# Optimization experiments

Measured on AMD Instinct MI355X. Metric: run time of the kernel, lower is better.

Reference implementation:

```python
import jax, jax.numpy as jnp
import numpy as np

B, S, C, H = 2, 2048, 512, 16
D = C // H  # 32
SQRT_DIM = float(np.sqrt(C))  # module scales by sqrt(in_channels), not sqrt(dim)


def setup_inputs() -> dict:
    key = jax.random.key(0)
    ks = jax.random.split(key, 16)
    sc = 1.0 / np.sqrt(C)
    f32 = jnp.float32
    return {
        "q": jax.random.normal(ks[0], (B, S, C), f32),
        "k": jax.random.normal(ks[1], (B, S, C), f32),
        "v": jax.random.normal(ks[2], (B, S, C), f32),
        "pos_embedding": jax.random.normal(ks[3], (B, S, C), f32),
        "Wq": jax.random.normal(ks[4], (C, C), f32) * sc,
        "bq": jnp.zeros((C,), f32),
        "Wk": jax.random.normal(ks[5], (C, C), f32) * sc,
        "bk": jnp.zeros((C,), f32),
        "Wv": jax.random.normal(ks[6], (C, C), f32) * sc,
        "bv": jnp.zeros((C,), f32),
        "Wp": jax.random.normal(ks[7], (C, C), f32) * sc,  # pos_proj has no bias
        "u_bias": jax.random.normal(ks[8], (H, D), f32) * 0.1,
        "v_bias": jax.random.normal(ks[9], (H, D), f32) * 0.1,
        "Wo": jax.random.normal(ks[10], (C, C), f32) * sc,
        "bo": jnp.zeros((C,), f32),
    }


def _skew(pos_score):
    # Transformer-XL pad-shift trick: [B,H,S1,S2] -> relative-shifted scores
    b, h, s1, s2 = pos_score.shape
    zeros = jnp.zeros((b, h, s1, 1), pos_score.dtype)
    padded = jnp.concatenate([zeros, pos_score], axis=-1)  # [b,h,s1,s2+1]
    padded = padded.reshape(b, h, s2 + 1, s1)
    return padded[:, :, 1:].reshape(b, h, s1, s2)


def reference(q, k, v, pos_embedding, Wq, bq, Wk, bk, Wv, bv, Wp, u_bias, v_bias, Wo, bo):
    query = (q @ Wq.T + bq).reshape(B, S, H, D)      # [B,S,H,D]
    key_ = (k @ Wk.T + bk).reshape(B, S, H, D)
    value = (v @ Wv.T + bv).reshape(B, S, H, D)
    pos = (pos_embedding @ Wp.T).reshape(B, S, H, D)
    content = jnp.einsum('bshd,bthd->bhst', query + u_bias, key_)   # [B,H,S,S]
    pos_score = _skew(jnp.einsum('bshd,bthd->bhst', query + v_bias, pos))
    score = (content + pos_score) / SQRT_DIM
    attn = jax.nn.softmax(score, axis=-1)            # dropout_p=0 (eval)
    context = jnp.einsum('bhst,bthd->bshd', attn, value).reshape(B, S, C)
    return context @ Wo.T + bo
```

## Files before the change

### kernel.cpp

```cpp
#include <hip/hip_runtime.h>
#include <math.h>

#define S_ 2048
#define C_ 512
#define H_ 16
#define D_ 32
#define B_ 2
#define M_ (B_ * S_)
#define RSCALE 0.04419417382415922f

typedef __attribute__((ext_vector_type(8))) short bf16x8;
typedef __attribute__((ext_vector_type(4))) float f32x4;

__device__ inline unsigned short f2bf(float f) {
  unsigned u = __builtin_bit_cast(unsigned, f);
  u += 0x7FFFu + ((u >> 16) & 1u);
  return (unsigned short)(u >> 16);
}

__global__ __launch_bounds__(256) void split_x(
    const float* __restrict__ q, const float* __restrict__ k,
    const float* __restrict__ v, const float* __restrict__ pe,
    short* __restrict__ xh, short* __restrict__ xl) {
  const int z = blockIdx.y;
  const float* src = z == 0 ? q : z == 1 ? k : z == 2 ? v : pe;
  const size_t off = (size_t)z * M_ * C_;
  const size_t i = ((size_t)blockIdx.x * 256 + threadIdx.x) * 4;
  float4 f = *(const float4*)(src + i);
  float ff[4] = {f.x, f.y, f.z, f.w};
  ushort4 hv, lv;
  unsigned short* ph = (unsigned short*)&hv;
  unsigned short* pl = (unsigned short*)&lv;
#pragma unroll
  for (int e = 0; e < 4; ++e) {
    unsigned u = __builtin_bit_cast(unsigned, ff[e]);
    unsigned hi = u & 0xffff0000u;
    ph[e] = (unsigned short)(hi >> 16);
    pl[e] = f2bf(ff[e] - __builtin_bit_cast(float, hi));
  }
  *(ushort4*)(xh + off + i) = hv;
  *(ushort4*)(xl + off + i) = lv;
}

__global__ __launch_bounds__(256) void split_w(
    const float* __restrict__ w0, const float* __restrict__ w1,
    const float* __restrict__ w2, const float* __restrict__ w3,
    const float* __restrict__ w4, short* __restrict__ wh,
    short* __restrict__ wl) {
  const int z = blockIdx.y;
  const float* src = z == 0 ? w0 : z == 1 ? w1 : z == 2 ? w2 : z == 3 ? w3 : w4;
  const size_t off = (size_t)z * C_ * C_;
  const size_t i = ((size_t)blockIdx.x * 256 + threadIdx.x) * 4;
  float4 f = *(const float4*)(src + i);
  float ff[4] = {f.x, f.y, f.z, f.w};
  ushort4 hv, lv;
  unsigned short* ph = (unsigned short*)&hv;
  unsigned short* pl = (unsigned short*)&lv;
#pragma unroll
  for (int e = 0; e < 4; ++e) {
    unsigned u = __builtin_bit_cast(unsigned, ff[e]);
    unsigned hi = u & 0xffff0000u;
    ph[e] = (unsigned short)(hi >> 16);
    pl[e] = f2bf(ff[e] - __builtin_bit_cast(float, hi));
  }
  *(ushort4*)(wh + off + i) = hv;
  *(ushort4*)(wl + off + i) = lv;
}

__device__ __forceinline__ void gemm_core(
    const short* __restrict__ Xh, const short* __restrict__ Xl,
    const short* __restrict__ Wh, const short* __restrict__ Wl,
    const float* bias, const float* bias2, const float* bias3,
    float* __restrict__ Of, short* __restrict__ Ob, short* __restrict__ Ob2,
    int mode) {
  __shared__ __align__(16) short LAh[2][64 * 72];
  __shared__ __align__(16) short LAl[2][64 * 72];
  __shared__ __align__(16) short LBh[2][64 * 72];
  __shared__ __align__(16) short LBl[2][64 * 72];
  const int tid = threadIdx.x;
  const int w = tid >> 6, lane = tid & 63, col = lane & 15, quad = lane >> 4;
  const int bm = blockIdx.y * 64, bn = blockIdx.x * 64;
  const f32x4 zc = {0.f, 0.f, 0.f, 0.f};
  f32x4 acc[4] = {zc, zc, zc, zc};

  uint4 rah[2], ral[2], rbh[2], rbl[2];
  const int r0 = tid >> 3, c0 = (tid & 7) * 8;
  const int r1 = (tid + 256) >> 3, c1 = c0;
#define LOAD_REGS(k0)                                                     \
  {                                                                       \
    rah[0] = *(const uint4*)(Xh + (size_t)(bm + r0) * C_ + (k0) + c0);    \
    ral[0] = *(const uint4*)(Xl + (size_t)(bm + r0) * C_ + (k0) + c0);    \
    rbh[0] = *(const uint4*)(Wh + (size_t)(bn + r0) * C_ + (k0) + c0);    \
    rbl[0] = *(const uint4*)(Wl + (size_t)(bn + r0) * C_ + (k0) + c0);    \
    rah[1] = *(const uint4*)(Xh + (size_t)(bm + r1) * C_ + (k0) + c1);    \
    ral[1] = *(const uint4*)(Xl + (size_t)(bm + r1) * C_ + (k0) + c1);    \
    rbh[1] = *(const uint4*)(Wh + (size_t)(bn + r1) * C_ + (k0) + c1);    \
    rbl[1] = *(const uint4*)(Wl + (size_t)(bn + r1) * C_ + (k0) + c1);    \
  }
#define STORE_LDS(buf)                                                    \
  {                                                                       \
    *(uint4*)&LAh[buf][r0 * 72 + c0] = rah[0];                            \
    *(uint4*)&LAl[buf][r0 * 72 + c0] = ral[0];                            \
    *(uint4*)&LBh[buf][r0 * 72 + c0] = rbh[0];                            \
    *(uint4*)&LBl[buf][r0 * 72 + c0] = rbl[0];                            \
    *(uint4*)&LAh[buf][r1 * 72 + c1] = rah[1];                            \
    *(uint4*)&LAl[buf][r1 * 72 + c1] = ral[1];                            \
    *(uint4*)&LBh[buf][r1 * 72 + c1] = rbh[1];                            \
    *(uint4*)&LBl[buf][r1 * 72 + c1] = rbl[1];                            \
  }
  LOAD_REGS(0)
  STORE_LDS(0)
  for (int it = 0; it < 8; ++it) {
    __syncthreads();
    if (it < 7) LOAD_REGS((it + 1) * 64)
    const int buf = it & 1;
#pragma unroll
    for (int ks = 0; ks < 2; ++ks) {
      const int ko = ks * 32 + quad * 8;
      const bf16x8 ah = *(const bf16x8*)&LAh[buf][(16 * w + col) * 72 + ko];
      const bf16x8 al = *(const bf16x8*)&LAl[buf][(16 * w + col) * 72 + ko];
#pragma unroll
      for (int j = 0; j < 4; ++j) {
        const bf16x8 bh = *(const bf16x8*)&LBh[buf][(16 * j + col) * 72 + ko];
        const bf16x8 bl = *(const bf16x8*)&LBl[buf][(16 * j + col) * 72 + ko];
        acc[j] = __builtin_amdgcn_mfma_f32_16x16x32_bf16(ah, bh, acc[j], 0, 0, 0);
        acc[j] = __builtin_amdgcn_mfma_f32_16x16x32_bf16(ah, bl, acc[j], 0, 0, 0);
        acc[j] = __builtin_amdgcn_mfma_f32_16x16x32_bf16(al, bh, acc[j], 0, 0, 0);
      }
    }
    if (it < 7) STORE_LDS(1 - buf)
  }
#undef LOAD_REGS
#undef STORE_LDS
#pragma unroll
  for (int j = 0; j < 4; ++j) {
    const int gn = bn + 16 * j + col;
#pragma unroll
    for (int r = 0; r < 4; ++r) {
      const int gm = bm + 16 * w + quad * 4 + r;
      const float a = acc[j][r];
      if (mode == 0) {
        Of[(size_t)gm * C_ + gn] = a + (bias ? bias[gn] : 0.0f);
      } else if (mode == 1) {
        const int h = gn >> 5, d0 = gn & 31;
        const int bb = gm >> 11, s = gm & (S_ - 1);
        const size_t base = ((size_t)(bb * H_ + h) * S_ + s) * D_ + d0;
        const float val = a + bias[gn];
        Ob[base] = (short)f2bf(val + bias2[gn]);
        Ob2[base] = (short)f2bf(val + bias3[gn]);
      } else if (mode == 2) {
        const int h = gn >> 5, d0 = gn & 31;
        const int bb = gm >> 11, s = gm & (S_ - 1);
        Ob[((size_t)(bb * H_ + h) * S_ + s) * D_ + d0] =
            (short)f2bf(a + (bias ? bias[gn] : 0.0f));
      } else {
        const int h = gn >> 5, d0 = gn & 31;
        const int bb = gm >> 11, s = gm & (S_ - 1);
        Ob[((size_t)(bb * H_ + h) * D_ + d0) * S_ + s] =
            (short)f2bf(a + (bias ? bias[gn] : 0.0f));
      }
    }
  }
}

__global__ __launch_bounds__(256, 2) void proj4(
    const short* __restrict__ XH, const short* __restrict__ XL,
    const short* __restrict__ WH, const short* __restrict__ WL,
    const float* bq, const float* bkk, const float* bvv,
    const float* ub, const float* vb,
    short* QU, short* QV, short* Kb, short* Vt, short* POS) {
  const int z = blockIdx.z;
  const size_t MC = (size_t)M_ * C_, WC = (size_t)C_ * C_;
  const short* xh = XH + z * MC;
  const short* xl = XL + z * MC;
  const short* wh = WH + z * WC;
  const short* wl = WL + z * WC;
  const float* b1 = z == 0 ? bq : z == 1 ? bkk : z == 2 ? bvv : nullptr;
  const int mode = z == 0 ? 1 : z == 2 ? 3 : 2;
  short* ob = z == 0 ? QU : z == 1 ? Kb : z == 2 ? Vt : POS;
  short* ob2 = z == 0 ? QV : nullptr;
  gemm_core(xh, xl, wh, wl, b1, z == 0 ? ub : nullptr, z == 0 ? vb : nullptr,
            nullptr, ob, ob2, mode);
}

__global__ __launch_bounds__(256, 2) void gemm_out(
    const short* __restrict__ CTXh, const short* __restrict__ CTXl,
    const short* __restrict__ WH, const short* __restrict__ WL,
    const float* bo, float* __restrict__ out) {
  const size_t WC = (size_t)C_ * C_;
  gemm_core(CTXh, CTXl, WH + 4 * WC, WL + 4 * WC, bo, nullptr, nullptr,
            out, nullptr, nullptr, 0);
}

__global__ __launch_bounds__(256, 4) void attn_mfma(
    const short* __restrict__ QU, const short* __restrict__ QV,
    const short* __restrict__ Kb, const short* __restrict__ Vt,
    const short* __restrict__ POSb, short* __restrict__ CTXh,
    short* __restrict__ CTXl) {
  __shared__ float PB[64 * 128];
  __shared__ short Pl[64 * 64];
  const int tid = threadIdx.x;
  const int w = tid >> 6;
  const int lane = tid & 63;
  const int col = lane & 15;
  const int quad = lane >> 4;
  const int m0 = blockIdx.x * 64;
  const int bh = blockIdx.y;
  const int b = bh >> 4, h = bh & 15;

  const short* QUh = QU + (size_t)bh * S_ * D_;
  const short* QVh = QV + (size_t)bh * S_ * D_;
  const short* Kh = Kb + (size_t)bh * S_ * D_;
  const short* Vh = Vt + (size_t)bh * D_ * S_;
  const short* Ph = POSb + (size_t)bh * S_ * D_;

  const int arow = m0 + 16 * w + col;
  const bf16x8 aQU = *(const bf16x8*)(QUh + (size_t)arow * D_ + quad * 8);
  const bf16x8 aQVA = *(const bf16x8*)(QVh + (size_t)arow * D_ + quad * 8);
  const bf16x8 aQVB = *(const bf16x8*)(QVh + (size_t)(arow + 1) * D_ + quad * 8);

  const f32x4 zc = {0.f, 0.f, 0.f, 0.f};
  const bf16x8 zb = {0, 0, 0, 0, 0, 0, 0, 0};
  f32x4 ctxa0 = zc, ctxa1 = zc;
  float lpart[4] = {0.f, 0.f, 0.f, 0.f};
  const int mi0 = 16 * w + 4 * quad;

  for (int ch = 0; ch < 32; ++ch) {
    const int n0 = ch * 64;
    const int dnm = n0 - m0;
    f32x4 sc[4];
#pragma unroll
    for (int j = 0; j < 4; ++j) {
      bf16x8 bk = *(const bf16x8*)(Kh + (size_t)(n0 + 16 * j + col) * D_ + quad * 8);
      sc[j] = __builtin_amdgcn_mfma_f32_16x16x32_bf16(aQU, bk, zc, 0, 0, 0);
    }
    if (dnm <= 63) {
      const int tA0 = S_ - 64 + dnm;
#pragma unroll
      for (int j = 0; j < 8; ++j) {
        const int t = tA0 + 16 * j + col;
        bf16x8 bp = *(const bf16x8*)(Ph + (long)t * D_ + quad * 8);
        if (t >= S_) bp = zb;
        f32x4 c = __builtin_amdgcn_mfma_f32_16x16x32_bf16(aQVA, bp, zc, 0, 0, 0);
#pragma unroll
        for (int r = 0; r < 4; ++r) {
          const int mi = mi0 + r;
          const int cc = (16 * j + col) ^ (((mi & 4) << 2) ^ ((mi & 3) << 3));
          PB[mi * 128 + cc] = c[r];
        }
      }
      __syncthreads();
#pragma unroll
      for (int j = 0; j < 4; ++j)
#pragma unroll
        for (int r = 0; r < 4; ++r) {
          const int mi = mi0 + r;
          const int nj = 16 * j + col;
          if (dnm + nj - mi <= 0) {
            const int idx = (nj - mi + 63) ^ (((mi & 4) << 2) ^ ((mi & 3) << 3));
            sc[j][r] += PB[mi * 128 + idx];
          }
        }
    }
    if (dnm >= -61) {
      __syncthreads();
      const int tB0 = dnm - 65;
#pragma unroll
      for (int j = 0; j < 8; ++j) {
        const int t = tB0 + 16 * j + col;
        bf16x8 bp = *(const bf16x8*)(Ph + (long)t * D_ + quad * 8);
        if (t < 0) bp = zb;
        f32x4 c = __builtin_amdgcn_mfma_f32_16x16x32_bf16(aQVB, bp, zc, 0, 0, 0);
#pragma unroll
        for (int r = 0; r < 4; ++r) {
          const int mi = mi0 + r;
          const int cc = (16 * j + col) ^ (((mi & 4) << 2) ^ ((mi & 3) << 3));
          PB[mi * 128 + cc] = c[r];
        }
      }
      __syncthreads();
#pragma unroll
      for (int j = 0; j < 4; ++j)
#pragma unroll
        for (int r = 0; r < 4; ++r) {
          const int mi = mi0 + r;
          const int nj = 16 * j + col;
          if (dnm + nj - mi >= 2) {
            const int idx = (nj - mi + 63) ^ (((mi & 4) << 2) ^ ((mi & 3) << 3));
            sc[j][r] += PB[mi * 128 + idx];
          }
        }
    }
    __syncthreads();
#pragma unroll
    for (int j = 0; j < 4; ++j)
#pragma unroll
      for (int r = 0; r < 4; ++r) {
        const float p = __expf(sc[j][r] * RSCALE);
        lpart[r] += p;
        const int mi = mi0 + r;
        const int cc = (16 * j + col) ^ ((mi & 7) << 3);
        Pl[mi * 64 + cc] = (short)f2bf(p);
      }
    __syncthreads();
    const int prow = 16 * w + col;
    const int psw = (prow & 7) << 3;
#pragma unroll
    for (int k0 = 0; k0 < 2; ++k0) {
      const bf16x8 ap = *(const bf16x8*)(&Pl[prow * 64 + ((k0 * 32 + quad * 8) ^ psw)]);
      bf16x8 bv0 = *(const bf16x8*)(Vh + (size_t)col * S_ + n0 + k0 * 32 + quad * 8);
      ctxa0 = __builtin_amdgcn_mfma_f32_16x16x32_bf16(ap, bv0, ctxa0, 0, 0, 0);
      bf16x8 bv1 = *(const bf16x8*)(Vh + (size_t)(16 + col) * S_ + n0 + k0 * 32 + quad * 8);
      ctxa1 = __builtin_amdgcn_mfma_f32_16x16x32_bf16(ap, bv1, ctxa1, 0, 0, 0);
    }
  }
#pragma unroll
  for (int r = 0; r < 4; ++r) {
    float s = lpart[r];
    s += __shfl_xor(s, 1);
    s += __shfl_xor(s, 2);
    s += __shfl_xor(s, 4);
    s += __shfl_xor(s, 8);
    lpart[r] = 1.0f / s;
  }
  const int mrow = m0 + mi0;
#pragma unroll
  for (int r = 0; r < 4; ++r) {
    const size_t obase = ((size_t)(b * S_ + mrow + r)) * C_ + h * D_;
    const float v0 = ctxa0[r] * lpart[r];
    const float v1 = ctxa1[r] * lpart[r];
    const unsigned u0 = __builtin_bit_cast(unsigned, v0) & 0xffff0000u;
    const unsigned u1 = __builtin_bit_cast(unsigned, v1) & 0xffff0000u;
    CTXh[obase + col] = (short)(u0 >> 16);
    CTXl[obase + col] = (short)f2bf(v0 - __builtin_bit_cast(float, u0));
    CTXh[obase + 16 + col] = (short)(u1 >> 16);
    CTXl[obase + 16 + col] = (short)f2bf(v1 - __builtin_bit_cast(float, u1));
  }
}

extern "C" void kernel_launch(void* const* d_in, const int* in_sizes, int n_in,
                              void* d_out, int out_size, void* d_ws, size_t ws_size,
                              hipStream_t stream) {
  (void)in_sizes; (void)n_in; (void)out_size; (void)ws_size;
  const float* q = (const float*)d_in[0];
  const float* k = (const float*)d_in[1];
  const float* v = (const float*)d_in[2];
  const float* pe = (const float*)d_in[3];
  const float* Wq = (const float*)d_in[4];
  const float* bq = (const float*)d_in[5];
  const float* Wk = (const float*)d_in[6];
  const float* bk = (const float*)d_in[7];
  const float* Wv = (const float*)d_in[8];
  const float* bv = (const float*)d_in[9];
  const float* Wp = (const float*)d_in[10];
  const float* ub = (const float*)d_in[11];
  const float* vb = (const float*)d_in[12];
  const float* Wo = (const float*)d_in[13];
  const float* bo = (const float*)d_in[14];
  float* out = (float*)d_out;

  const size_t MC = (size_t)M_ * C_;
  const size_t WC = (size_t)C_ * C_;
  short* XH = (short*)d_ws;
  short* XL = XH + 4 * MC;
  short* WH = XL + 4 * MC;
  short* WL = WH + 5 * WC;
  short* QUb = WL + 5 * WC;
  short* QVb = QUb + MC;
  short* Kbb = QVb + MC;
  short* Vtb = Kbb + MC;
  short* POSB = Vtb + MC;
  short* CTXh = POSB + MC;
  short* CTXl = CTXh + MC;

  split_x<<<dim3(2048, 4), 256, 0, stream>>>(q, k, v, pe, XH, XL);
  split_w<<<dim3(256, 5), 256, 0, stream>>>(Wq, Wk, Wv, Wp, Wo, WH, WL);
  proj4<<<dim3(8, 64, 4), 256, 0, stream>>>(XH, XL, WH, WL, bq, bk, bv, ub, vb,
                                            QUb, QVb, Kbb, Vtb, POSB);
  attn_mfma<<<dim3(S_ / 64, B_ * H_), 256, 0, stream>>>(QUb, QVb, Kbb, Vtb, POSB,
                                                        CTXh, CTXl);
  gemm_out<<<dim3(8, 64), 256, 0, stream>>>(CTXh, CTXl, WH, WL, bo, out);
}
```

Baseline: 371.1 us.

## Use single-bf16 input projections and LDS-free direct-load GEMMs with 128-row tiles

The four input projections drop the hi/lo bf16 split and run as one bf16 MFMA per product, which halves conversion writes and projection loads and cuts MFMA count by three. Both projection and output GEMMs drop shared-memory double buffering and load operands straight from global memory into registers, with each wave now covering 32 rows. The output projection keeps the three-term split for accuracy. The risk is lower accuracy in Q/K/V/pos, and uncoalesced global loads that depend on cache reuse instead of LDS.

```diff
diff --git a/kernel.cpp b/kernel.cpp
--- a/kernel.cpp
+++ b/kernel.cpp
@@ -18,178 +18,158 @@
   return (unsigned short)(u >> 16);
 }
 
-__global__ __launch_bounds__(256) void split_x(
+__global__ __launch_bounds__(256) void split_x4(
     const float* __restrict__ q, const float* __restrict__ k,
     const float* __restrict__ v, const float* __restrict__ pe,
-    short* __restrict__ xh, short* __restrict__ xl) {
+    short* __restrict__ xb) {
   const int z = blockIdx.y;
   const float* src = z == 0 ? q : z == 1 ? k : z == 2 ? v : pe;
   const size_t off = (size_t)z * M_ * C_;
   const size_t i = ((size_t)blockIdx.x * 256 + threadIdx.x) * 4;
   float4 f = *(const float4*)(src + i);
   float ff[4] = {f.x, f.y, f.z, f.w};
-  ushort4 hv, lv;
+  ushort4 hv;
   unsigned short* ph = (unsigned short*)&hv;
-  unsigned short* pl = (unsigned short*)&lv;
-#pragma unroll
-  for (int e = 0; e < 4; ++e) {
-    unsigned u = __builtin_bit_cast(unsigned, ff[e]);
-    unsigned hi = u & 0xffff0000u;
-    ph[e] = (unsigned short)(hi >> 16);
-    pl[e] = f2bf(ff[e] - __builtin_bit_cast(float, hi));
-  }
-  *(ushort4*)(xh + off + i) = hv;
-  *(ushort4*)(xl + off + i) = lv;
+#pragma unroll
+  for (int e = 0; e < 4; ++e) ph[e] = f2bf(ff[e]);
+  *(ushort4*)(xb + off + i) = hv;
 }
 
 __global__ __launch_bounds__(256) void split_w(
     const float* __restrict__ w0, const float* __restrict__ w1,
     const float* __restrict__ w2, const float* __restrict__ w3,
-    const float* __restrict__ w4, short* __restrict__ wh,
-    short* __restrict__ wl) {
+    const float* __restrict__ w4, short* __restrict__ wb,
+    short* __restrict__ woh, short* __restrict__ wol) {
   const int z = blockIdx.y;
   const float* src = z == 0 ? w0 : z == 1 ? w1 : z == 2 ? w2 : z == 3 ? w3 : w4;
-  const size_t off = (size_t)z * C_ * C_;
   const size_t i = ((size_t)blockIdx.x * 256 + threadIdx.x) * 4;
   float4 f = *(const float4*)(src + i);
   float ff[4] = {f.x, f.y, f.z, f.w};
-  ushort4 hv, lv;
-  unsigned short* ph = (unsigned short*)&hv;
-  unsigned short* pl = (unsigned short*)&lv;
-#pragma unroll
-  for (int e = 0; e < 4; ++e) {
-    unsigned u = __builtin_bit_cast(unsigned, ff[e]);
-    unsigned hi = u & 0xffff0000u;
-    ph[e] = (unsigned short)(hi >> 16);
-    pl[e] = f2bf(ff[e] - __builtin_bit_cast(float, hi));
-  }
-  *(ushort4*)(wh + off + i) = hv;
-  *(ushort4*)(wl + off + i) = lv;
-}
-
-__device__ __forceinline__ void gemm_core(
-    const short* __restrict__ Xh, const short* __restrict__ Xl,
-    const short* __restrict__ Wh, const short* __restrict__ Wl,
-    const float* bias, const float* bias2, const float* bias3,
-    float* __restrict__ Of, short* __restrict__ Ob, short* __restrict__ Ob2,
-    int mode) {
-  __shared__ __align__(16) short LAh[2][64 * 72];
-  __shared__ __align__(16) short LAl[2][64 * 72];
-  __shared__ __align__(16) short LBh[2][64 * 72];
-  __shared__ __align__(16) short LBl[2][64 * 72];
+  if (z < 4) {
+    const size_t off = (size_t)z * C_ * C_;
+    ushort4 hv;
+    unsigned short* ph = (unsigned short*)&hv;
+#pragma unroll
+    for (int e = 0; e < 4; ++e) ph[e] = f2bf(ff[e]);
+    *(ushort4*)(wb + off + i) = hv;
+  } else {
+    ushort4 hv, lv;
+    unsigned short* ph = (unsigned short*)&hv;
+    unsigned short* pl = (unsigned short*)&lv;
+#pragma unroll
+    for (int e = 0; e < 4; ++e) {
+      unsigned u = __builtin_bit_cast(unsigned, ff[e]);
+      unsigned hi = u & 0xffff0000u;
+      ph[e] = (unsigned short)(hi >> 16);
+      pl[e] = f2bf(ff[e] - __builtin_bit_cast(float, hi));
+    }
+    *(ushort4*)(woh + i) = hv;
+    *(ushort4*)(wol + i) = lv;
+  }
+}
+
+__global__ __launch_bounds__(256) void proj4(
+    const short* __restrict__ XB, const short* __restrict__ W4,
+    const float* __restrict__ bq, const float* __restrict__ bkk,
+    const float* __restrict__ bvv, const float* __restrict__ ub,
+    const float* __restrict__ vb, short* __restrict__ QU,
+    short* __restrict__ QV, short* __restrict__ Kb, short* __restrict__ Vt,
+    short* __restrict__ POS) {
+  const int z = blockIdx.z;
+  const short* X = XB + (size_t)z * M_ * C_;
+  const short* W = W4 + (size_t)z * C_ * C_;
   const int tid = threadIdx.x;
   const int w = tid >> 6, lane = tid & 63, col = lane & 15, quad = lane >> 4;
-  const int bm = blockIdx.y * 64, bn = blockIdx.x * 64;
+  const int bm = blockIdx.y * 128, bn = blockIdx.x * 64;
   const f32x4 zc = {0.f, 0.f, 0.f, 0.f};
-  f32x4 acc[4] = {zc, zc, zc, zc};
-
-  uint4 rah[2], ral[2], rbh[2], rbl[2];
-  const int r0 = tid >> 3, c0 = (tid & 7) * 8;
-  const int r1 = (tid + 256) >> 3, c1 = c0;
-#define LOAD_REGS(k0)                                                     \
-  {                                                                       \
-    rah[0] = *(const uint4*)(Xh + (size_t)(bm + r0) * C_ + (k0) + c0);    \
-    ral[0] = *(const uint4*)(Xl + (size_t)(bm + r0) * C_ + (k0) + c0);    \
-    rbh[0] = *(const uint4*)(Wh + (size_t)(bn + r0) * C_ + (k0) + c0);    \
-    rbl[0] = *(const uint4*)(Wl + (size_t)(bn + r0) * C_ + (k0) + c0);    \
-    rah[1] = *(const uint4*)(Xh + (size_t)(bm + r1) * C_ + (k0) + c1);    \
-    ral[1] = *(const uint4*)(Xl + (size_t)(bm + r1) * C_ + (k0) + c1);    \
-    rbh[1] = *(const uint4*)(Wh + (size_t)(bn + r1) * C_ + (k0) + c1);    \
-    rbl[1] = *(const uint4*)(Wl + (size_t)(bn + r1) * C_ + (k0) + c1);    \
-  }
-#define STORE_LDS(buf)                                                    \
-  {                                                                       \
-    *(uint4*)&LAh[buf][r0 * 72 + c0] = rah[0];                            \
-    *(uint4*)&LAl[buf][r0 * 72 + c0] = ral[0];                            \
-    *(uint4*)&LBh[buf][r0 * 72 + c0] = rbh[0];                            \
-    *(uint4*)&LBl[buf][r0 * 72 + c0] = rbl[0];                            \
-    *(uint4*)&LAh[buf][r1 * 72 + c1] = rah[1];                            \
-    *(uint4*)&LAl[buf][r1 * 72 + c1] = ral[1];                            \
-    *(uint4*)&LBh[buf][r1 * 72 + c1] = rbh[1];                            \
-    *(uint4*)&LBl[buf][r1 * 72 + c1] = rbl[1];                            \
-  }
-  LOAD_REGS(0)
-  STORE_LDS(0)
-  for (int it = 0; it < 8; ++it) {
-    __syncthreads();
-    if (it < 7) LOAD_REGS((it + 1) * 64)
-    const int buf = it & 1;
-#pragma unroll
-    for (int ks = 0; ks < 2; ++ks) {
-      const int ko = ks * 32 + quad * 8;
-      const bf16x8 ah = *(const bf16x8*)&LAh[buf][(16 * w + col) * 72 + ko];
-      const bf16x8 al = *(const bf16x8*)&LAl[buf][(16 * w + col) * 72 + ko];
-#pragma unroll
-      for (int j = 0; j < 4; ++j) {
-        const bf16x8 bh = *(const bf16x8*)&LBh[buf][(16 * j + col) * 72 + ko];
-        const bf16x8 bl = *(const bf16x8*)&LBl[buf][(16 * j + col) * 72 + ko];
-        acc[j] = __builtin_amdgcn_mfma_f32_16x16x32_bf16(ah, bh, acc[j], 0, 0, 0);
-        acc[j] = __builtin_amdgcn_mfma_f32_16x16x32_bf16(ah, bl, acc[j], 0, 0, 0);
-        acc[j] = __builtin_amdgcn_mfma_f32_16x16x32_bf16(al, bh, acc[j], 0, 0, 0);
-      }
-    }
-    if (it < 7) STORE_LDS(1 - buf)
-  }
-#undef LOAD_REGS
-#undef STORE_LDS
-#pragma unroll
-  for (int j = 0; j < 4; ++j) {
-    const int gn = bn + 16 * j + col;
-#pragma unroll
-    for (int r = 0; r < 4; ++r) {
-      const int gm = bm + 16 * w + quad * 4 + r;
-      const float a = acc[j][r];
-      if (mode == 0) {
-        Of[(size_t)gm * C_ + gn] = a + (bias ? bias[gn] : 0.0f);
-      } else if (mode == 1) {
-        const int h = gn >> 5, d0 = gn & 31;
+  f32x4 acc[2][4] = {{zc, zc, zc, zc}, {zc, zc, zc, zc}};
+  const short* Xr0 = X + (size_t)(bm + 32 * w + col) * C_ + quad * 8;
+  const short* Xr1 = Xr0 + 16 * C_;
+  const short* Wr = W + (size_t)(bn + col) * C_ + quad * 8;
+#pragma unroll 4
+  for (int kt = 0; kt < 16; ++kt) {
+    const int k = kt * 32;
+    const bf16x8 a0 = *(const bf16x8*)(Xr0 + k);
+    const bf16x8 a1 = *(const bf16x8*)(Xr1 + k);
+#pragma unroll
+    for (int j = 0; j < 4; ++j) {
+      const bf16x8 b = *(const bf16x8*)(Wr + (size_t)(16 * j) * C_ + k);
+      acc[0][j] = __builtin_amdgcn_mfma_f32_16x16x32_bf16(a0, b, acc[0][j], 0, 0, 0);
+      acc[1][j] = __builtin_amdgcn_mfma_f32_16x16x32_bf16(a1, b, acc[1][j], 0, 0, 0);
+    }
+  }
+  const float* b1 = z == 0 ? bq : z == 1 ? bkk : z == 2 ? bvv : nullptr;
+#pragma unroll
+  for (int mt = 0; mt < 2; ++mt) {
+#pragma unroll
+    for (int j = 0; j < 4; ++j) {
+      const int gn = bn + 16 * j + col;
+      const int h = gn >> 5, d0 = gn & 31;
+#pragma unroll
+      for (int r = 0; r < 4; ++r) {
+        const int gm = bm + 32 * w + 16 * mt + quad * 4 + r;
         const int bb = gm >> 11, s = gm & (S_ - 1);
-        const size_t base = ((size_t)(bb * H_ + h) * S_ + s) * D_ + d0;
-        const float val = a + bias[gn];
-        Ob[base] = (short)f2bf(val + bias2[gn]);
-        Ob2[base] = (short)f2bf(val + bias3[gn]);
-      } else if (mode == 2) {
-        const int h = gn >> 5, d0 = gn & 31;
-        const int bb = gm >> 11, s = gm & (S_ - 1);
-        Ob[((size_t)(bb * H_ + h) * S_ + s) * D_ + d0] =
-            (short)f2bf(a + (bias ? bias[gn] : 0.0f));
-      } else {
-        const int h = gn >> 5, d0 = gn & 31;
-        const int bb = gm >> 11, s = gm & (S_ - 1);
-        Ob[((size_t)(bb * H_ + h) * D_ + d0) * S_ + s] =
-            (short)f2bf(a + (bias ? bias[gn] : 0.0f));
-      }
-    }
-  }
-}
-
-__global__ __launch_bounds__(256, 2) void proj4(
-    const short* __restrict__ XH, const short* __restrict__ XL,
-    const short* __restrict__ WH, const short* __restrict__ WL,
-    const float* bq, const float* bkk, const float* bvv,
-    const float* ub, const float* vb,
-    short* QU, short* QV, short* Kb, short* Vt, short* POS) {
-  const int z = blockIdx.z;
-  const size_t MC = (size_t)M_ * C_, WC = (size_t)C_ * C_;
-  const short* xh = XH + z * MC;
-  const short* xl = XL + z * MC;
-  const short* wh = WH + z * WC;
-  const short* wl = WL + z * WC;
-  const float* b1 = z == 0 ? bq : z == 1 ? bkk : z == 2 ? bvv : nullptr;
-  const int mode = z == 0 ? 1 : z == 2 ? 3 : 2;
-  short* ob = z == 0 ? QU : z == 1 ? Kb : z == 2 ? Vt : POS;
-  short* ob2 = z == 0 ? QV : nullptr;
-  gemm_core(xh, xl, wh, wl, b1, z == 0 ? ub : nullptr, z == 0 ? vb : nullptr,
-            nullptr, ob, ob2, mode);
-}
-
-__global__ __launch_bounds__(256, 2) void gemm_out(
+        const float a = acc[mt][j][r] + (b1 ? b1[gn] : 0.0f);
+        if (z == 0) {
+          const size_t base = ((size_t)(bb * H_ + h) * S_ + s) * D_ + d0;
+          QU[base] = (short)f2bf(a + ub[gn]);
+          QV[base] = (short)f2bf(a + vb[gn]);
+        } else if (z == 1) {
+          Kb[((size_t)(bb * H_ + h) * S_ + s) * D_ + d0] = (short)f2bf(a);
+        } else if (z == 2) {
+          Vt[((size_t)(bb * H_ + h) * D_ + d0) * S_ + s] = (short)f2bf(a);
+        } else {
+          POS[((size_t)(bb * H_ + h) * S_ + s) * D_ + d0] = (short)f2bf(a);
+        }
+      }
+    }
+  }
+}
+
+__global__ __launch_bounds__(256) void gemm_out(
     const short* __restrict__ CTXh, const short* __restrict__ CTXl,
-    const short* __restrict__ WH, const short* __restrict__ WL,
-    const float* bo, float* __restrict__ out) {
-  const size_t WC = (size_t)C_ * C_;
-  gemm_core(CTXh, CTXl, WH + 4 * WC, WL + 4 * WC, bo, nullptr, nullptr,
-            out, nullptr, nullptr, 0);
+    const short* __restrict__ WOh, const short* __restrict__ WOl,
+    const float* __restrict__ bo, float* __restrict__ out) {
+  const int tid = threadIdx.x;
+  const int w = tid >> 6, lane = tid & 63, col = lane & 15, quad = lane >> 4;
+  const int bm = blockIdx.y * 128, bn = blockIdx.x * 64;
+  const f32x4 zc = {0.f, 0.f, 0.f, 0.f};
+  f32x4 acc[2][4] = {{zc, zc, zc, zc}, {zc, zc, zc, zc}};
+  const size_t a0off = (size_t)(bm + 32 * w + col) * C_ + quad * 8;
+  const size_t a1off = a0off + (size_t)16 * C_;
+  const size_t boff = (size_t)(bn + col) * C_ + quad * 8;
+#pragma unroll 2
+  for (int kt = 0; kt < 16; ++kt) {
+    const int k = kt * 32;
+    const bf16x8 ah0 = *(const bf16x8*)(CTXh + a0off + k);
+    const bf16x8 al0 = *(const bf16x8*)(CTXl + a0off + k);
+    const bf16x8 ah1 = *(const bf16x8*)(CTXh + a1off + k);
+    const bf16x8 al1 = *(const bf16x8*)(CTXl + a1off + k);
+#pragma unroll
+    for (int j = 0; j < 4; ++j) {
+      const size_t bo_ = boff + (size_t)(16 * j) * C_ + k;
+      const bf16x8 bh = *(const bf16x8*)(WOh + bo_);
+      const bf16x8 bl = *(const bf16x8*)(WOl + bo_);
+      acc[0][j] = __builtin_amdgcn_mfma_f32_16x16x32_bf16(ah0, bh, acc[0][j], 0, 0, 0);
+      acc[0][j] = __builtin_amdgcn_mfma_f32_16x16x32_bf16(ah0, bl, acc[0][j], 0, 0, 0);
+      acc[0][j] = __builtin_amdgcn_mfma_f32_16x16x32_bf16(al0, bh, acc[0][j], 0, 0, 0);
+      acc[1][j] = __builtin_amdgcn_mfma_f32_16x16x32_bf16(ah1, bh, acc[1][j], 0, 0, 0);
+      acc[1][j] = __builtin_amdgcn_mfma_f32_16x16x32_bf16(ah1, bl, acc[1][j], 0, 0, 0);
+      acc[1][j] = __builtin_amdgcn_mfma_f32_16x16x32_bf16(al1, bh, acc[1][j], 0, 0, 0);
+    }
+  }
+#pragma unroll
+  for (int mt = 0; mt < 2; ++mt) {
+#pragma unroll
+    for (int j = 0; j < 4; ++j) {
+      const int gn = bn + 16 * j + col;
+#pragma unroll
+      for (int r = 0; r < 4; ++r) {
+        const int gm = bm + 32 * w + 16 * mt + quad * 4 + r;
+        out[(size_t)gm * C_ + gn] = acc[mt][j][r] + bo[gn];
+      }
+    }
+  }
 }
 
 __global__ __launch_bounds__(256, 4) void attn_mfma(
@@ -361,11 +341,11 @@
 
   const size_t MC = (size_t)M_ * C_;
   const size_t WC = (size_t)C_ * C_;
-  short* XH = (short*)d_ws;
-  short* XL = XH + 4 * MC;
-  short* WH = XL + 4 * MC;
-  short* WL = WH + 5 * WC;
-  short* QUb = WL + 5 * WC;
+  short* XB = (short*)d_ws;
+  short* W4 = XB + 4 * MC;
+  short* WOh = W4 + 4 * WC;
+  short* WOl = WOh + WC;
+  short* QUb = WOl + WC;
   short* QVb = QUb + MC;
   short* Kbb = QVb + MC;
   short* Vtb = Kbb + MC;
@@ -373,11 +353,11 @@
   short* CTXh = POSB + MC;
   short* CTXl = CTXh + MC;
 
-  split_x<<<dim3(2048, 4), 256, 0, stream>>>(q, k, v, pe, XH, XL);
-  split_w<<<dim3(256, 5), 256, 0, stream>>>(Wq, Wk, Wv, Wp, Wo, WH, WL);
-  proj4<<<dim3(8, 64, 4), 256, 0, stream>>>(XH, XL, WH, WL, bq, bk, bv, ub, vb,
+  split_x4<<<dim3(2048, 4), 256, 0, stream>>>(q, k, v, pe, XB);
+  split_w<<<dim3(256, 5), 256, 0, stream>>>(Wq, Wk, Wv, Wp, Wo, W4, WOh, WOl);
+  proj4<<<dim3(8, 32, 4), 256, 0, stream>>>(XB, W4, bq, bk, bv, ub, vb,
                                             QUb, QVb, Kbb, Vtb, POSB);
   attn_mfma<<<dim3(S_ / 64, B_ * H_), 256, 0, stream>>>(QUb, QVb, Kbb, Vtb, POSB,
                                                         CTXh, CTXl);
-  gemm_out<<<dim3(8, 64), 256, 0, stream>>>(CTXh, CTXl, WH, WL, bo, out);
-}
+  gemm_out<<<dim3(8, 32), 256, 0, stream>>>(CTXh, CTXl, WOh, WOl, bo, out);
+}
```

Result: slower. 381.3 us (+2.7%).
